# Kernel tuning notes

Hardware: AMD Instinct MI355X
Metric: run time of the kernel (lower is better)

The kernel has to match this reference:

```python
import jax, jax.numpy as jnp
import numpy as np

EPS = 1e-6


def _rms_norm(x, w):
    # RMSNorm over last dim in fp32, like Qwen3RMSNorm
    x32 = x.astype(jnp.float32)
    var = jnp.mean(x32 * x32, axis=-1, keepdims=True)
    return (x32 * jax.lax.rsqrt(var + EPS)).astype(x.dtype) * w


def _rotate_half(x):
    h = x.shape[-1] // 2
    return jnp.concatenate([-x[..., h:], x[..., :h]], axis=-1)


def setup_inputs() -> dict:
    key = jax.random.key(0)
    ks = jax.random.split(key, 8)
    B, S, HID = 1, 8192, 1024
    H, HKV, D = 16, 8, 128
    n_seg = 8
    hidden_states = jax.random.normal(ks[0], (B, S, HID), dtype=jnp.float32)
    cu_seqlens = jnp.arange(n_seg + 1, dtype=jnp.int32) * (S // n_seg)
    # multimodal RoPE tables: two position streams, each [B, S, D]
    inv_freq = 1.0 / (1e6 ** (jnp.arange(0, D, 2, dtype=jnp.float32) / D))
    pos = jnp.arange(S, dtype=jnp.float32)
    ang0 = pos[:, None] * inv_freq[None, :]            # [S, D/2]
    ang1 = (pos[:, None] * 0.5) * inv_freq[None, :]    # second stream
    def tab(a):
        return jnp.concatenate([a, a], axis=-1)[None]   # [1, S, D]
    cos = jnp.stack([tab(jnp.cos(ang0)), tab(jnp.cos(ang1))], axis=0)  # [2,1,S,D]
    sin = jnp.stack([tab(jnp.sin(ang0)), tab(jnp.sin(ang1))], axis=0)
    sd = 0.02
    Wq = jax.random.normal(ks[1], (H * D, HID), dtype=jnp.float32) * sd
    Wk = jax.random.normal(ks[2], (HKV * D, HID), dtype=jnp.float32) * sd
    Wv = jax.random.normal(ks[3], (HKV * D, HID), dtype=jnp.float32) * sd
    Wo = jax.random.normal(ks[4], (HID, H * D), dtype=jnp.float32) * sd
    q_norm_w = 1.0 + jax.random.normal(ks[5], (D,), dtype=jnp.float32) * sd
    k_norm_w = 1.0 + jax.random.normal(ks[6], (D,), dtype=jnp.float32) * sd
    return {"hidden_states": hidden_states, "cu_seqlens": cu_seqlens,
            "cos": cos, "sin": sin, "Wq": Wq, "Wk": Wk, "Wv": Wv, "Wo": Wo,
            "q_norm_w": q_norm_w, "k_norm_w": k_norm_w}


def reference(hidden_states, cu_seqlens, cos, sin, Wq, Wk, Wv, Wo, q_norm_w, k_norm_w):
    B, S, _ = hidden_states.shape
    D = q_norm_w.shape[0]
    H = Wq.shape[0] // D
    HKV = Wk.shape[0] // D
    groups = H // HKV
    n_seg = cu_seqlens.shape[0] - 1   # equal-length segments (static)
    L = S // n_seg
    scaling = D ** -0.5

    # projections -> [B, H(kv), S, D]
    q = (hidden_states @ Wq.T).reshape(B, S, H, D).transpose(0, 2, 1, 3)
    k = (hidden_states @ Wk.T).reshape(B, S, HKV, D).transpose(0, 2, 1, 3)
    v = (hidden_states @ Wv.T).reshape(B, S, HKV, D).transpose(0, 2, 1, 3)

    q = _rms_norm(q, q_norm_w)
    k = _rms_norm(k, k_norm_w)

    # multimodal RoPE: interleave the two streams across the two half-dims
    half = D // 2
    cos_e = jnp.concatenate([cos[0, ..., :half], cos[1, ..., half:]], axis=-1)[:, None]  # [B,1,S,D]
    sin_e = jnp.concatenate([sin[0, ..., :half], sin[1, ..., half:]], axis=-1)[:, None]
    q = q * cos_e + _rotate_half(q) * sin_e
    k = k * cos_e + _rotate_half(k) * sin_e

    # GQA: repeat kv heads
    k = jnp.repeat(k, groups, axis=1)
    v = jnp.repeat(v, groups, axis=1)

    # block-diagonal attention over cu_seqlens segments (equal-length -> reshape)
    qb = q.reshape(B, H, n_seg, L, D)
    kb = k.reshape(B, H, n_seg, L, D)
    vb = v.reshape(B, H, n_seg, L, D)
    scores = jnp.einsum('bhnld,bhnmd->bhnlm', qb, kb) * scaling
    probs = jax.nn.softmax(scores, axis=-1)
    ob = jnp.einsum('bhnlm,bhnmd->bhnld', probs, vb)
    out = ob.reshape(B, H, S, D).transpose(0, 2, 1, 3).reshape(B, S, H * D)
    return out @ Wo.T
```

## Files before the change

kernel.cpp:

```cpp
#include <hip/hip_runtime.h>

#define S_LEN 8192
#define HID   1024
#define NH    16
#define NKV   8
#define HD    128
#define LSEG  1024

typedef float  f4  __attribute__((ext_vector_type(4)));
typedef _Float16 h4 __attribute__((ext_vector_type(4)));
typedef _Float16 h8 __attribute__((ext_vector_type(8)));

__device__ __forceinline__ void gl_lds16(const void* g, void* l) {
  __builtin_amdgcn_global_load_lds((const __attribute__((address_space(1))) void*)g,
                                   (__attribute__((address_space(3))) void*)l, 16, 0, 0);
}

__device__ __forceinline__ h8 ld8u(const _Float16* p) {
  h4 a = *(const h4*)p;
  h4 b = *(const h4*)(p + 4);
  return __builtin_shufflevector(a, b, 0, 1, 2, 3, 4, 5, 6, 7);
}

template <int CTRL>
__device__ __forceinline__ float dppf(float v) {
  return __builtin_bit_cast(float,
      __builtin_amdgcn_mov_dpp(__builtin_bit_cast(int, v), CTRL, 0xF, 0xF, true));
}
__device__ __forceinline__ float red16_max(float x) {
  x = fmaxf(x, dppf<0xB1>(x));
  x = fmaxf(x, dppf<0x4E>(x));
  x = fmaxf(x, dppf<0x141>(x));
  x = fmaxf(x, dppf<0x140>(x));
  return x;
}
__device__ __forceinline__ float red16_sum(float x) {
  x += dppf<0xB1>(x);
  x += dppf<0x4E>(x);
  x += dppf<0x141>(x);
  x += dppf<0x140>(x);
  return x;
}
__device__ __forceinline__ float bcast16(float v) {
  return __builtin_bit_cast(float,
      __builtin_amdgcn_ds_swizzle(__builtin_bit_cast(int, v), 0x0010));
}

__global__ void convert_kernel(const float* __restrict__ hid, const float* __restrict__ wq,
                               const float* __restrict__ wk, const float* __restrict__ wv,
                               const float* __restrict__ wo,
                               _Float16* __restrict__ hid16, _Float16* __restrict__ wqkv,
                               _Float16* __restrict__ wo16) {
  const int total4 = 3670016;
  for (int i = blockIdx.x * blockDim.x + threadIdx.x; i < total4; i += gridDim.x * blockDim.x) {
    int i4 = i * 4;
    const float* src; _Float16* dst;
    if      (i4 <  8388608) { src = hid + i4;              dst = hid16 + i4; }
    else if (i4 < 10485760) { src = wq + (i4 -  8388608);  dst = wqkv + (i4 - 8388608); }
    else if (i4 < 11534336) { src = wk + (i4 - 10485760);  dst = wqkv + 2097152 + (i4 - 10485760); }
    else if (i4 < 12582912) { src = wv + (i4 - 11534336);  dst = wqkv + 3145728 + (i4 - 11534336); }
    else                    { src = wo + (i4 - 12582912);  dst = wo16 + (i4 - 12582912); }
    f4 x = *(const f4*)src;
    h4 y; y[0]=(_Float16)x[0]; y[1]=(_Float16)x[1]; y[2]=(_Float16)x[2]; y[3]=(_Float16)x[3];
    *(h4*)dst = y;
  }
}

template <int FUSED>
__global__ __launch_bounds__(256, 3)
void gemm_kernel(const _Float16* __restrict__ A, const _Float16* __restrict__ B,
                 float* __restrict__ Cout, int K, int N,
                 const float* __restrict__ cosp, const float* __restrict__ sinp,
                 const float* __restrict__ qnw, const float* __restrict__ knw,
                 _Float16* __restrict__ q16, _Float16* __restrict__ k16,
                 _Float16* __restrict__ v16T) {
  __shared__ __align__(16) char smem[32768];

  constexpr int GX  = FUSED ? 32 : 8;
  constexpr int NWG = FUSED ? 2048 : 512;
  const int lin = blockIdx.y * GX + blockIdx.x;
  const int swz = (lin & 7) * (NWG >> 3) + (lin >> 3);
  const int bx = swz & (GX - 1), by = swz / GX;

  const int tid = threadIdx.x, w = tid >> 6, ln = tid & 63;
  const int l15 = ln & 15, l4 = ln >> 4;
  const int m0 = by * 128, n0 = bx * 128;
  const int sg_row = ln >> 2, sg_cho = (ln & 3) * 8;

  f4 acc[2][8] = {};

  for (int k0 = 0; k0 < K; k0 += 64) {
    __syncthreads();
#pragma unroll
    for (int r = 0; r < 2; r++) {
      int ch = r * 4 + w;
#pragma unroll
      for (int u = 0; u < 2; u++) {
        gl_lds16(A + (size_t)(m0 + ch * 16 + sg_row) * K + k0 + u * 32 + sg_cho,
                 smem + u * 8192 + ch * 1024);
        gl_lds16(B + (size_t)(n0 + ch * 16 + sg_row) * K + k0 + u * 32 + sg_cho,
                 smem + 16384 + u * 8192 + ch * 1024);
      }
    }
    __syncthreads();
#pragma unroll
    for (int u = 0; u < 2; u++) {
      const _Float16* As = (const _Float16*)(smem + u * 8192);
      const _Float16* Bs = (const _Float16*)(smem + 16384 + u * 8192);
      h8 af[2], bf[8];
#pragma unroll
      for (int mt = 0; mt < 2; mt++) af[mt] = *(const h8*)(As + (w * 32 + mt * 16 + l15) * 32 + l4 * 8);
#pragma unroll
      for (int nt = 0; nt < 8; nt++) bf[nt] = *(const h8*)(Bs + (nt * 16 + l15) * 32 + l4 * 8);
#pragma unroll
      for (int mt = 0; mt < 2; mt++)
#pragma unroll
        for (int nt = 0; nt < 8; nt++)
          acc[mt][nt] = __builtin_amdgcn_mfma_f32_16x16x32_f16(af[mt], bf[nt], acc[mt][nt], 0, 0, 0);
    }
  }

  if (!FUSED) {
#pragma unroll
    for (int mt = 0; mt < 2; mt++)
#pragma unroll
      for (int rg = 0; rg < 4; rg++) {
        int row = m0 + w * 32 + mt * 16 + l4 * 4 + rg;
#pragma unroll
        for (int nt = 0; nt < 8; nt++)
          Cout[(size_t)row * N + n0 + nt * 16 + l15] = acc[mt][nt][rg];
      }
    return;
  } else {
    const int head = bx;
    if (head < 24) {
      const float* nw = (head < 16) ? qnw : knw;
      const float hs = (head < 16) ? 0.12751734f : 1.0f;
      _Float16* base = (head < 16) ? q16 + (size_t)head * S_LEN * HD
                                   : k16 + (size_t)(head - 16) * S_LEN * HD;
      float nwv[8];
#pragma unroll
      for (int nt = 0; nt < 8; nt++) nwv[nt] = nw[nt * 16 + l15];
#pragma unroll
      for (int mt = 0; mt < 2; mt++)
#pragma unroll
        for (int rg = 0; rg < 4; rg++) {
          const int row = m0 + w * 32 + mt * 16 + l4 * 4 + rg;
          float ss = 0.f;
#pragma unroll
          for (int nt = 0; nt < 8; nt++) ss += acc[mt][nt][rg] * acc[mt][nt][rg];
          ss = red16_sum(ss);
          const float sc = rsqrtf(ss * 0.0078125f + 1e-6f);
#pragma unroll
          for (int nt = 0; nt < 8; nt++) {
            const int c = nt * 16 + l15;
            const int str = (nt >= 4) ? 1048576 : 0;
            float x  = acc[mt][nt][rg] * sc * nwv[nt];
            float xp = acc[mt][nt ^ 4][rg] * sc * nwv[nt ^ 4];
            float ce = cosp[str + row * HD + c];
            float se = sinp[str + row * HD + c];
            float rot = (nt >= 4) ? xp : -xp;
            base[(size_t)row * HD + c] = (_Float16)((x * ce + rot * se) * hs);
          }
        }
    } else {
      _Float16* vb = v16T + (size_t)(head - 24) * S_LEN * HD;
#pragma unroll
      for (int mt = 0; mt < 2; mt++)
#pragma unroll
        for (int nt = 0; nt < 8; nt++) {
          h4 hv;
#pragma unroll
          for (int rg = 0; rg < 4; rg++) hv[rg] = (_Float16)acc[mt][nt][rg];
          *(h4*)&vb[(size_t)(nt * 16 + l15) * S_LEN + m0 + w * 32 + mt * 16 + l4 * 4] = hv;
        }
    }
  }
}

__global__ __launch_bounds__(256, 2)
void attn_kernel(const _Float16* __restrict__ q16, const _Float16* __restrict__ k16,
                 const _Float16* __restrict__ vT, _Float16* __restrict__ ao16) {
  const int bid = blockIdx.x;
  const int xcd = bid & 7, slot = bid >> 3;
  const int grp = xcd * 8 + (slot >> 4);
  const int mem = slot & 15;
  const int g = grp >> 3, hkv = grp & 7;
  const int tq = mem & 7, h = hkv * 2 + (mem >> 3);

  const int tid = threadIdx.x, w = tid >> 6, ln = tid & 63;
  const int l15 = ln & 15, l4 = ln >> 4;

  __shared__ _Float16 Qs[128 * 132];
  __shared__ _Float16 KP[128 * 68];
  __shared__ _Float16 Vt[144 * 68];

  const _Float16* qsrc = q16 + ((size_t)h * S_LEN + g * LSEG + tq * 128) * HD;
#pragma unroll
  for (int i = 0; i < 8; i++) {
    int c = tid + 256 * i, row = c >> 4, o = c & 15;
    uint4 v = *(const uint4*)(qsrc + row * HD + o * 8);
    *(uint2*)&Qs[row * 132 + o * 8]     = make_uint2(v.x, v.y);
    *(uint2*)&Qs[row * 132 + o * 8 + 4] = make_uint2(v.z, v.w);
  }
  if (tid < 68) {
    Vt[128 * 68 + tid] = (_Float16)1.0f;
#pragma unroll
    for (int r = 129; r < 144; r++) Vt[r * 68 + tid] = (_Float16)0.0f;
  }

  f4 O[2][9] = {};
  float mr[2][4];
#pragma unroll
  for (int mt = 0; mt < 2; mt++)
#pragma unroll
    for (int rg = 0; rg < 4; rg++) mr[mt][rg] = -1e30f;

  const size_t kbase = ((size_t)hkv * S_LEN + g * LSEG) * HD;
  const size_t vbase = (size_t)hkv * S_LEN * HD + (size_t)g * LSEG;

  const int krow = tid >> 4, ko = tid & 15;
  const int vd   = tid >> 3, vo = tid & 7;

  uint4 kr[4], vr[4];
#pragma unroll
  for (int i = 0; i < 4; i++) {
    kr[i] = *(const uint4*)(k16 + kbase + (size_t)(krow + 16 * i) * HD + ko * 8);
    vr[i] = *(const uint4*)(vT + vbase + (size_t)(vd + 32 * i) * S_LEN + vo * 8);
  }
#pragma unroll
  for (int i = 0; i < 4; i++) {
    int row = krow + 16 * i;
    *(uint2*)&KP[row * 132 + ko * 8]     = make_uint2(kr[i].x, kr[i].y);
    *(uint2*)&KP[row * 132 + ko * 8 + 4] = make_uint2(kr[i].z, kr[i].w);
    int d = vd + 32 * i;
    *(uint2*)&Vt[d * 68 + vo * 8]     = make_uint2(vr[i].x, vr[i].y);
    *(uint2*)&Vt[d * 68 + vo * 8 + 4] = make_uint2(vr[i].z, vr[i].w);
  }

  for (int j = 0; j < 16; j++) {
    __syncthreads();

    const int jn = (j + 1) & 15;
#pragma unroll
    for (int i = 0; i < 4; i++) {
      kr[i] = *(const uint4*)(k16 + kbase + (size_t)(jn * 64 + krow + 16 * i) * HD + ko * 8);
      vr[i] = *(const uint4*)(vT + vbase + (size_t)(vd + 32 * i) * S_LEN + jn * 64 + vo * 8);
    }

    f4 s[2][4] = {};
    __builtin_amdgcn_s_setprio(1);
#pragma unroll
    for (int kk = 0; kk < 4; kk++) {
      h8 a0 = ld8u(Qs + (w * 32 + l15) * 132 + kk * 32 + l4 * 8);
      h8 a1 = ld8u(Qs + (w * 32 + 16 + l15) * 132 + kk * 32 + l4 * 8);
#pragma unroll
      for (int nt = 0; nt < 4; nt++) {
        h8 b = ld8u(KP + (nt * 16 + l15) * 132 + kk * 32 + l4 * 8);
        s[0][nt] = __builtin_amdgcn_mfma_f32_16x16x32_f16(a0, b, s[0][nt], 0, 0, 0);
        s[1][nt] = __builtin_amdgcn_mfma_f32_16x16x32_f16(a1, b, s[1][nt], 0, 0, 0);
      }
    }
    __builtin_amdgcn_s_setprio(0);

    bool nd = false;
#pragma unroll
    for (int mt = 0; mt < 2; mt++)
#pragma unroll
      for (int rg = 0; rg < 4; rg++) {
        float thr = mr[mt][rg] + 8.f;
        nd = nd || (s[mt][0][rg] > thr) || (s[mt][1][rg] > thr) ||
                   (s[mt][2][rg] > thr) || (s[mt][3][rg] > thr);
      }
    const bool needr = __any((int)nd) != 0;
    float al[2][4];
    if (needr) {
#pragma unroll
      for (int mt = 0; mt < 2; mt++)
#pragma unroll
        for (int rg = 0; rg < 4; rg++) {
          float m = fmaxf(fmaxf(s[mt][0][rg], s[mt][1][rg]), fmaxf(s[mt][2][rg], s[mt][3][rg]));
          m = red16_max(m);
          float mnew = fmaxf(mr[mt][rg], m);
          al[mt][rg] = exp2f(mr[mt][rg] - mnew);
          mr[mt][rg] = mnew;
        }
    }
#pragma unroll
    for (int mt = 0; mt < 2; mt++)
#pragma unroll
      for (int rg = 0; rg < 4; rg++)
#pragma unroll
        for (int nt = 0; nt < 4; nt++)
          s[mt][nt][rg] = exp2f(s[mt][nt][rg] - mr[mt][rg]);

    __syncthreads();
#pragma unroll
    for (int mt = 0; mt < 2; mt++)
#pragma unroll
      for (int nt = 0; nt < 4; nt++)
#pragma unroll
        for (int rg = 0; rg < 4; rg++)
          KP[(w * 32 + mt * 16 + l4 * 4 + rg) * 68 + nt * 16 + l15] = (_Float16)s[mt][nt][rg];
    if (needr) {
#pragma unroll
      for (int mt = 0; mt < 2; mt++)
#pragma unroll
        for (int d8 = 0; d8 < 9; d8++)
#pragma unroll
          for (int rg = 0; rg < 4; rg++) O[mt][d8][rg] *= al[mt][rg];
    }

    __builtin_amdgcn_s_setprio(1);
#pragma unroll
    for (int kk = 0; kk < 2; kk++) {
      h8 a0 = ld8u(KP + (w * 32 + l15) * 68 + kk * 32 + l4 * 8);
      h8 a1 = ld8u(KP + (w * 32 + 16 + l15) * 68 + kk * 32 + l4 * 8);
#pragma unroll
      for (int d8 = 0; d8 < 9; d8++) {
        h8 b = ld8u(Vt + (d8 * 16 + l15) * 68 + kk * 32 + l4 * 8);
        O[0][d8] = __builtin_amdgcn_mfma_f32_16x16x32_f16(a0, b, O[0][d8], 0, 0, 0);
        O[1][d8] = __builtin_amdgcn_mfma_f32_16x16x32_f16(a1, b, O[1][d8], 0, 0, 0);
      }
    }
    __builtin_amdgcn_s_setprio(0);

    __syncthreads();
#pragma unroll
    for (int i = 0; i < 4; i++) {
      int row = krow + 16 * i;
      *(uint2*)&KP[row * 132 + ko * 8]     = make_uint2(kr[i].x, kr[i].y);
      *(uint2*)&KP[row * 132 + ko * 8 + 4] = make_uint2(kr[i].z, kr[i].w);
      int d = vd + 32 * i;
      *(uint2*)&Vt[d * 68 + vo * 8]     = make_uint2(vr[i].x, vr[i].y);
      *(uint2*)&Vt[d * 68 + vo * 8 + 4] = make_uint2(vr[i].z, vr[i].w);
    }
  }

  const size_t obase = (size_t)(g * LSEG + tq * 128);
#pragma unroll
  for (int mt = 0; mt < 2; mt++)
#pragma unroll
    for (int rg = 0; rg < 4; rg++) {
      float inv = 1.f / bcast16(O[mt][8][rg]);
#pragma unroll
      for (int d8 = 0; d8 < 8; d8++)
        ao16[(obase + w * 32 + mt * 16 + l4 * 4 + rg) * 2048 + h * HD + d8 * 16 + l15] =
            (_Float16)(O[mt][d8][rg] * inv);
    }
}

extern "C" void kernel_launch(void* const* d_in, const int* in_sizes, int n_in,
                              void* d_out, int out_size, void* d_ws, size_t ws_size,
                              hipStream_t stream) {
  const float* hid  = (const float*)d_in[0];
  const float* cosp = (const float*)d_in[2];
  const float* sinp = (const float*)d_in[3];
  const float* wq   = (const float*)d_in[4];
  const float* wk   = (const float*)d_in[5];
  const float* wv   = (const float*)d_in[6];
  const float* wo   = (const float*)d_in[7];
  const float* qnw  = (const float*)d_in[8];
  const float* knw  = (const float*)d_in[9];
  float* out = (float*)d_out;

  _Float16* hid16 = (_Float16*)d_ws;
  _Float16* wqkv  = hid16 + 8388608;
  _Float16* wo16  = wqkv + 4194304;
  _Float16* q16   = wo16 + 2097152;
  _Float16* k16   = q16 + 16777216;
  _Float16* v16T  = k16 + 8388608;
  _Float16* ao16  = v16T + 8388608;

  convert_kernel<<<dim3(1024), dim3(256), 0, stream>>>(hid, wq, wk, wv, wo, hid16, wqkv, wo16);
  gemm_kernel<1><<<dim3(32, 64), dim3(256), 0, stream>>>(hid16, wqkv, nullptr, 1024, 4096,
                                                         cosp, sinp, qnw, knw, q16, k16, v16T);
  attn_kernel<<<dim3(1024), dim3(256), 0, stream>>>(q16, k16, v16T, ao16);
  gemm_kernel<0><<<dim3(8, 64), dim3(256), 0, stream>>>(ao16, wo16, out, 2048, 1024,
                                                        nullptr, nullptr, nullptr, nullptr,
                                                        nullptr, nullptr, nullptr);
}
```

Baseline: 389.6 us.

## Keep Q in registers and double-buffer K/V LDS to cut barriers

Q fragments now live in registers instead of LDS. K and V tiles are double-buffered, and the P tile reuses the next V buffer, with each warp writing its own rows, so the loop drops from three barriers to one. The row-sum column of ones now comes from a register constant B operand instead of padded LDS rows, and the V layout per thread changes so each warp writes only the P rows it owns. This cuts LDS traffic and synchronisation but adds register pressure (the qf fragments) under launch_bounds(256,2).

```diff
diff --git a/kernel.cpp b/kernel.cpp
--- a/kernel.cpp
+++ b/kernel.cpp
@@ -191,22 +191,22 @@
   const int tid = threadIdx.x, w = tid >> 6, ln = tid & 63;
   const int l15 = ln & 15, l4 = ln >> 4;
 
-  __shared__ _Float16 Qs[128 * 132];
-  __shared__ _Float16 KP[128 * 68];
-  __shared__ _Float16 Vt[144 * 68];
-
-  const _Float16* qsrc = q16 + ((size_t)h * S_LEN + g * LSEG + tq * 128) * HD;
-#pragma unroll
-  for (int i = 0; i < 8; i++) {
-    int c = tid + 256 * i, row = c >> 4, o = c & 15;
-    uint4 v = *(const uint4*)(qsrc + row * HD + o * 8);
-    *(uint2*)&Qs[row * 132 + o * 8]     = make_uint2(v.x, v.y);
-    *(uint2*)&Qs[row * 132 + o * 8 + 4] = make_uint2(v.z, v.w);
-  }
-  if (tid < 68) {
-    Vt[128 * 68 + tid] = (_Float16)1.0f;
-#pragma unroll
-    for (int r = 129; r < 144; r++) Vt[r * 68 + tid] = (_Float16)0.0f;
+  __shared__ _Float16 Kb[2][64 * 132];
+  __shared__ _Float16 Vb[2][128 * 68];
+
+  const _Float16* qsrc = q16 + ((size_t)h * S_LEN + g * LSEG + tq * 128 + w * 32) * HD;
+  h8 qf[2][4];
+#pragma unroll
+  for (int mt = 0; mt < 2; mt++)
+#pragma unroll
+    for (int kk = 0; kk < 4; kk++)
+      qf[mt][kk] = *(const h8*)(qsrc + (size_t)(mt * 16 + l15) * HD + kk * 32 + l4 * 8);
+
+  h8 onesB;
+  {
+    _Float16 ov = (l15 == 0) ? (_Float16)1.0f : (_Float16)0.0f;
+#pragma unroll
+    for (int jj = 0; jj < 8; jj++) onesB[jj] = ov;
   }
 
   f4 O[2][9] = {};
@@ -221,6 +221,7 @@
 
   const int krow = tid >> 4, ko = tid & 15;
   const int vd   = tid >> 3, vo = tid & 7;
+  const int vrow = w * 32 + (ln >> 1), vcol = (ln & 1) * 32;
 
   uint4 kr[4], vr[4];
 #pragma unroll
@@ -231,34 +232,40 @@
 #pragma unroll
   for (int i = 0; i < 4; i++) {
     int row = krow + 16 * i;
-    *(uint2*)&KP[row * 132 + ko * 8]     = make_uint2(kr[i].x, kr[i].y);
-    *(uint2*)&KP[row * 132 + ko * 8 + 4] = make_uint2(kr[i].z, kr[i].w);
+    *(uint2*)&Kb[0][row * 132 + ko * 8]     = make_uint2(kr[i].x, kr[i].y);
+    *(uint2*)&Kb[0][row * 132 + ko * 8 + 4] = make_uint2(kr[i].z, kr[i].w);
     int d = vd + 32 * i;
-    *(uint2*)&Vt[d * 68 + vo * 8]     = make_uint2(vr[i].x, vr[i].y);
-    *(uint2*)&Vt[d * 68 + vo * 8 + 4] = make_uint2(vr[i].z, vr[i].w);
+    *(uint2*)&Vb[0][d * 68 + vo * 8]     = make_uint2(vr[i].x, vr[i].y);
+    *(uint2*)&Vb[0][d * 68 + vo * 8 + 4] = make_uint2(vr[i].z, vr[i].w);
   }
 
   for (int j = 0; j < 16; j++) {
     __syncthreads();
-
-    const int jn = (j + 1) & 15;
-#pragma unroll
-    for (int i = 0; i < 4; i++) {
-      kr[i] = *(const uint4*)(k16 + kbase + (size_t)(jn * 64 + krow + 16 * i) * HD + ko * 8);
-      vr[i] = *(const uint4*)(vT + vbase + (size_t)(vd + 32 * i) * S_LEN + jn * 64 + vo * 8);
+    const int cur = j & 1, nxt = cur ^ 1;
+    const _Float16* Kc = Kb[cur];
+    const _Float16* Vc = Vb[cur];
+    _Float16* Pb = Vb[nxt];
+    _Float16* Kn = Kb[nxt];
+
+    if (j < 15) {
+      const int jn = j + 1;
+#pragma unroll
+      for (int i = 0; i < 4; i++)
+        kr[i] = *(const uint4*)(k16 + kbase + (size_t)(jn * 64 + krow + 16 * i) * HD + ko * 8);
+#pragma unroll
+      for (int c = 0; c < 4; c++)
+        vr[c] = *(const uint4*)(vT + vbase + (size_t)vrow * S_LEN + jn * 64 + vcol + c * 8);
     }
 
     f4 s[2][4] = {};
     __builtin_amdgcn_s_setprio(1);
 #pragma unroll
     for (int kk = 0; kk < 4; kk++) {
-      h8 a0 = ld8u(Qs + (w * 32 + l15) * 132 + kk * 32 + l4 * 8);
-      h8 a1 = ld8u(Qs + (w * 32 + 16 + l15) * 132 + kk * 32 + l4 * 8);
 #pragma unroll
       for (int nt = 0; nt < 4; nt++) {
-        h8 b = ld8u(KP + (nt * 16 + l15) * 132 + kk * 32 + l4 * 8);
-        s[0][nt] = __builtin_amdgcn_mfma_f32_16x16x32_f16(a0, b, s[0][nt], 0, 0, 0);
-        s[1][nt] = __builtin_amdgcn_mfma_f32_16x16x32_f16(a1, b, s[1][nt], 0, 0, 0);
+        h8 b = ld8u(Kc + (nt * 16 + l15) * 132 + kk * 32 + l4 * 8);
+        s[0][nt] = __builtin_amdgcn_mfma_f32_16x16x32_f16(qf[0][kk], b, s[0][nt], 0, 0, 0);
+        s[1][nt] = __builtin_amdgcn_mfma_f32_16x16x32_f16(qf[1][kk], b, s[1][nt], 0, 0, 0);
       }
     }
     __builtin_amdgcn_s_setprio(0);
@@ -294,14 +301,13 @@
         for (int nt = 0; nt < 4; nt++)
           s[mt][nt][rg] = exp2f(s[mt][nt][rg] - mr[mt][rg]);
 
-    __syncthreads();
 #pragma unroll
     for (int mt = 0; mt < 2; mt++)
 #pragma unroll
       for (int nt = 0; nt < 4; nt++)
 #pragma unroll
         for (int rg = 0; rg < 4; rg++)
-          KP[(w * 32 + mt * 16 + l4 * 4 + rg) * 68 + nt * 16 + l15] = (_Float16)s[mt][nt][rg];
+          Pb[(w * 32 + mt * 16 + l4 * 4 + rg) * 68 + nt * 16 + l15] = (_Float16)s[mt][nt][rg];
     if (needr) {
 #pragma unroll
       for (int mt = 0; mt < 2; mt++)
@@ -314,26 +320,31 @@
     __builtin_amdgcn_s_setprio(1);
 #pragma unroll
     for (int kk = 0; kk < 2; kk++) {
-      h8 a0 = ld8u(KP + (w * 32 + l15) * 68 + kk * 32 + l4 * 8);
-      h8 a1 = ld8u(KP + (w * 32 + 16 + l15) * 68 + kk * 32 + l4 * 8);
-#pragma unroll
-      for (int d8 = 0; d8 < 9; d8++) {
-        h8 b = ld8u(Vt + (d8 * 16 + l15) * 68 + kk * 32 + l4 * 8);
+      h8 a0 = ld8u(Pb + (w * 32 + l15) * 68 + kk * 32 + l4 * 8);
+      h8 a1 = ld8u(Pb + (w * 32 + 16 + l15) * 68 + kk * 32 + l4 * 8);
+#pragma unroll
+      for (int d8 = 0; d8 < 8; d8++) {
+        h8 b = ld8u(Vc + (d8 * 16 + l15) * 68 + kk * 32 + l4 * 8);
         O[0][d8] = __builtin_amdgcn_mfma_f32_16x16x32_f16(a0, b, O[0][d8], 0, 0, 0);
         O[1][d8] = __builtin_amdgcn_mfma_f32_16x16x32_f16(a1, b, O[1][d8], 0, 0, 0);
       }
+      O[0][8] = __builtin_amdgcn_mfma_f32_16x16x32_f16(a0, onesB, O[0][8], 0, 0, 0);
+      O[1][8] = __builtin_amdgcn_mfma_f32_16x16x32_f16(a1, onesB, O[1][8], 0, 0, 0);
     }
     __builtin_amdgcn_s_setprio(0);
 
-    __syncthreads();
-#pragma unroll
-    for (int i = 0; i < 4; i++) {
-      int row = krow + 16 * i;
-      *(uint2*)&KP[row * 132 + ko * 8]     = make_uint2(kr[i].x, kr[i].y);
-      *(uint2*)&KP[row * 132 + ko * 8 + 4] = make_uint2(kr[i].z, kr[i].w);
-      int d = vd + 32 * i;
-      *(uint2*)&Vt[d * 68 + vo * 8]     = make_uint2(vr[i].x, vr[i].y);
-      *(uint2*)&Vt[d * 68 + vo * 8 + 4] = make_uint2(vr[i].z, vr[i].w);
+    if (j < 15) {
+#pragma unroll
+      for (int i = 0; i < 4; i++) {
+        int row = krow + 16 * i;
+        *(uint2*)&Kn[row * 132 + ko * 8]     = make_uint2(kr[i].x, kr[i].y);
+        *(uint2*)&Kn[row * 132 + ko * 8 + 4] = make_uint2(kr[i].z, kr[i].w);
+      }
+#pragma unroll
+      for (int c = 0; c < 4; c++) {
+        *(uint2*)&Pb[vrow * 68 + vcol + c * 8]     = make_uint2(vr[c].x, vr[c].y);
+        *(uint2*)&Pb[vrow * 68 + vcol + c * 8 + 4] = make_uint2(vr[c].z, vr[c].w);
+      }
     }
   }
 
```

Result: faster. 366.2 us (-6.0%).
